# Kernel optimization log

Hardware: AMD Instinct MI355X
Metric: run time of the kernel (lower is better)

## Reference

```python
import jax, jax.numpy as jnp
import numpy as np

NEG_INF = -jnp.inf


def _bilinear_resize(x, out_h, out_w):
    """Matches torch F.interpolate(mode='bilinear', align_corners=False, antialias=False).
    x: [N, C, H, W] -> [N, C, out_h, out_w]."""
    N, C, H, W = x.shape

    def idx(in_s, out_s):
        scale = in_s / out_s
        src = jnp.maximum((jnp.arange(out_s, dtype=jnp.float32) + 0.5) * scale - 0.5, 0.0)
        i0 = jnp.floor(src).astype(jnp.int32)
        i1 = jnp.minimum(i0 + 1, in_s - 1)
        w = src - i0.astype(jnp.float32)
        return i0, i1, w

    y0, y1, wy = idx(H, out_h)
    x0, x1, wx = idx(W, out_w)
    # blend rows
    top = x[:, :, y0, :] * (1.0 - wy)[None, None, :, None] + x[:, :, y1, :] * wy[None, None, :, None]
    # blend cols
    out = top[:, :, :, x0] * (1.0 - wx)[None, None, None, :] + top[:, :, :, x1] * wx[None, None, None, :]
    return out


def _maxpool2(x):
    return jax.lax.reduce_window(x, NEG_INF, jax.lax.max,
                                 (1, 1, 2, 2), (1, 1, 2, 2), 'VALID')


def _lrelu(x):
    return jnp.where(x >= 0, x, 0.2 * x)


def setup_inputs() -> dict:
    key = jax.random.key(0)
    ks = jax.random.split(key, 6)
    N, C, H, W = 4, 32, 256, 256
    KS2 = 9
    psf = jax.random.normal(ks[0], (N, C, H, W), dtype=jnp.float32)
    featuremap = jax.random.normal(ks[1], (N, C, H, W), dtype=jnp.float32)
    w1 = jax.random.normal(ks[2], (C * KS2, C), dtype=jnp.float32) * 0.05
    b1 = jnp.zeros((C * KS2,), dtype=jnp.float32)
    ws = jax.random.normal(ks[3], (C * KS2, C), dtype=jnp.float32) * 0.05
    bs = jnp.zeros((C * KS2,), dtype=jnp.float32)
    return {"psf": psf, "featuremap": featuremap, "w1": w1, "b1": b1, "ws": ws, "bs": bs}


def reference(psf, featuremap, w1, b1, ws, bs):
    N, C, H, W = featuremap.shape
    KS = 3
    # psf branch: 1/4 bilinear -> maxpool2 -> KPResBlock (1x1 convs) -> x8 bilinear
    p = _bilinear_resize(psf, H // 4, W // 4)
    p = _maxpool2(p)                       # [N, C, H/8, W/8]
    identity = jnp.einsum('nchw,oc->nohw', p, ws) + bs[None, :, None, None]
    y = _lrelu(jnp.einsum('nchw,oc->nohw', p, w1) + b1[None, :, None, None]) + identity
    filt = _bilinear_resize(y, H, W)       # [N, C*9, H, W]
    # FAC: per-pixel dynamic 3x3 filter, fused (no materialized unfold)
    wflt = filt.reshape(N, C, KS * KS, H, W)
    padded = jnp.pad(featuremap, ((0, 0), (0, 0), (1, 1), (1, 1)))
    out = jnp.zeros((N, C, H, W), dtype=featuremap.dtype)
    for dy in range(KS):
        for dx in range(KS):
            out = out + padded[:, :, dy:dy + H, dx:dx + W] * wflt[:, :, dy * KS + dx]
    return out
```

## Files before the change

kernel.cpp:

```cpp
#include <hip/hip_runtime.h>

#define N_ 4
#define C_ 32
#define H_ 256
#define W_ 256
#define O_ 288
#define PH 32
#define P_ELEMS (N_*C_*PH*PH)
#define Y_ELEMS (N_*O_*PH*PH)
#define OUT_ELEMS (N_*C_*H_*W_)

__global__ __launch_bounds__(256) void k_downsample(
    const float* __restrict__ psf, float* __restrict__ p) {
  int tid = blockIdx.x * blockDim.x + threadIdx.x;
  if (tid >= P_ELEMS) return;
  int tx = tid & 31;
  int ty = (tid >> 5) & 31;
  int nc = tid >> 10;
  const float* x = psf + (size_t)nc * (H_ * W_);
  float m = -1e30f;
#pragma unroll
  for (int a = 0; a < 2; a++) {
#pragma unroll
    for (int b = 0; b < 2; b++) {
      int r0 = 8 * ty + 4 * a + 1;
      int c0 = 8 * tx + 4 * b;
      const float4 q0 = *(const float4*)(x + r0 * W_ + c0);
      const float4 q1 = *(const float4*)(x + (r0 + 1) * W_ + c0);
      float avg = 0.25f * (q0.y + q0.z + q1.y + q1.z);
      m = fmaxf(m, avg);
    }
  }
  p[tid] = m;
}

__global__ __launch_bounds__(256) void k_conv1x1(
    const float* __restrict__ p, const float* __restrict__ w1,
    const float* __restrict__ b1, const float* __restrict__ ws,
    const float* __restrict__ bs, float* __restrict__ y) {
  int bid = blockIdx.x;
  int n = bid / O_;
  int o = bid - n * O_;
  const float4* p4 = (const float4*)(p + (size_t)n * (C_ * PH * PH));
  const float* w1o = w1 + o * C_;
  const float* wso = ws + o * C_;
  float bb1 = b1[o];
  float bbs = bs[o];
  int t = threadIdx.x;
  float a1x = bb1, a1y = bb1, a1z = bb1, a1w = bb1;
  float a2x = bbs, a2y = bbs, a2z = bbs, a2w = bbs;
#pragma unroll
  for (int c = 0; c < C_; c++) {
    float4 pv = p4[c * 256 + t];
    float u1 = w1o[c], u2 = wso[c];
    a1x = fmaf(pv.x, u1, a1x); a1y = fmaf(pv.y, u1, a1y);
    a1z = fmaf(pv.z, u1, a1z); a1w = fmaf(pv.w, u1, a1w);
    a2x = fmaf(pv.x, u2, a2x); a2y = fmaf(pv.y, u2, a2y);
    a2z = fmaf(pv.z, u2, a2z); a2w = fmaf(pv.w, u2, a2w);
  }
  float4 r;
  r.x = ((a1x >= 0.f) ? a1x : 0.2f * a1x) + a2x;
  r.y = ((a1y >= 0.f) ? a1y : 0.2f * a1y) + a2y;
  r.z = ((a1z >= 0.f) ? a1z : 0.2f * a1z) + a2z;
  r.w = ((a1w >= 0.f) ? a1w : 0.2f * a1w) + a2w;
  ((float4*)(y + (size_t)bid * (PH * PH)))[t] = r;
}

__global__ __launch_bounds__(256) void k_fac(
    const float* __restrict__ fm, const float* __restrict__ y,
    float* __restrict__ out) {
  int bid = blockIdx.x;
  int work = (bid >> 3) + (bid & 7) * 256;
  int a = work & 15;
  int c = (work >> 4) & 31;
  int n = work >> 9;
  int t = threadIdx.x;
  int m = t & 31;
  int r = t >> 5;
  int h0 = (a << 4) + (r << 1);

  float sh0 = fmaxf(0.125f * (float)h0 - 0.4375f, 0.f);
  float sh1 = fmaxf(0.125f * (float)h0 - 0.3125f, 0.f);
  int y0 = (int)sh0;
  float wy0 = sh0 - (float)y0;
  float wy1 = sh1 - (float)y0;
  int y1 = min(y0 + 1, 31);

  const float* yb = y + ((size_t)(n * O_ + c * 9) << 10) + m;
  const float* yr0 = yb + (y0 << 5);
  const float* yr1 = yb + (y1 << 5);
  float tbA[9], tbB[9];
#pragma unroll
  for (int k = 0; k < 9; k++) {
    float t0 = yr0[k << 10];
    float u0 = yr1[k << 10];
    float d = u0 - t0;
    tbA[k] = fmaf(wy0, d, t0);
    tbB[k] = fmaf(wy1, d, t0);
  }
  int cm1 = max(m - 1, 0);
  int cp1 = min(m + 1, 31);

  const float* fb = fm + ((size_t)(n * C_ + c) << 16);

  float acc[16];
#pragma unroll
  for (int j = 0; j < 16; j++) acc[j] = 0.f;

#pragma unroll
  for (int i = 0; i < 4; i++) {
    int row = h0 - 1 + i;
    float fv[10];
    if (row >= 0 && row < 256) {
      const float* fr = fb + (row << 8) + (m << 3);
      float4 q0 = *(const float4*)(fr);
      float4 q1 = *(const float4*)(fr + 4);
      float left = __shfl(q1.w, cm1, 32);
      float right = __shfl(q0.x, cp1, 32);
      fv[0] = (m > 0) ? left : 0.f;
      fv[1] = q0.x; fv[2] = q0.y; fv[3] = q0.z; fv[4] = q0.w;
      fv[5] = q1.x; fv[6] = q1.y; fv[7] = q1.z; fv[8] = q1.w;
      fv[9] = (m < 31) ? right : 0.f;
    } else {
#pragma unroll
      for (int tt = 0; tt < 10; tt++) fv[tt] = 0.f;
    }
#pragma unroll
    for (int kx = 0; kx < 3; kx++) {
      if (i <= 2) {
        int k = 3 * i + kx;
        float tbm = tbA[k];
        float tbl = __shfl(tbm, cm1, 32);
        float tbr = __shfl(tbm, cp1, 32);
        float d0 = tbm - tbl;
        float d1 = tbr - tbm;
        acc[0] = fmaf(fv[0 + kx], fmaf(0.5625f, d0, tbl), acc[0]);
        acc[1] = fmaf(fv[1 + kx], fmaf(0.6875f, d0, tbl), acc[1]);
        acc[2] = fmaf(fv[2 + kx], fmaf(0.8125f, d0, tbl), acc[2]);
        acc[3] = fmaf(fv[3 + kx], fmaf(0.9375f, d0, tbl), acc[3]);
        acc[4] = fmaf(fv[4 + kx], fmaf(0.0625f, d1, tbm), acc[4]);
        acc[5] = fmaf(fv[5 + kx], fmaf(0.1875f, d1, tbm), acc[5]);
        acc[6] = fmaf(fv[6 + kx], fmaf(0.3125f, d1, tbm), acc[6]);
        acc[7] = fmaf(fv[7 + kx], fmaf(0.4375f, d1, tbm), acc[7]);
      }
      if (i >= 1) {
        int k = 3 * (i - 1) + kx;
        float tbm = tbB[k];
        float tbl = __shfl(tbm, cm1, 32);
        float tbr = __shfl(tbm, cp1, 32);
        float d0 = tbm - tbl;
        float d1 = tbr - tbm;
        acc[8]  = fmaf(fv[0 + kx], fmaf(0.5625f, d0, tbl), acc[8]);
        acc[9]  = fmaf(fv[1 + kx], fmaf(0.6875f, d0, tbl), acc[9]);
        acc[10] = fmaf(fv[2 + kx], fmaf(0.8125f, d0, tbl), acc[10]);
        acc[11] = fmaf(fv[3 + kx], fmaf(0.9375f, d0, tbl), acc[11]);
        acc[12] = fmaf(fv[4 + kx], fmaf(0.0625f, d1, tbm), acc[12]);
        acc[13] = fmaf(fv[5 + kx], fmaf(0.1875f, d1, tbm), acc[13]);
        acc[14] = fmaf(fv[6 + kx], fmaf(0.3125f, d1, tbm), acc[14]);
        acc[15] = fmaf(fv[7 + kx], fmaf(0.4375f, d1, tbm), acc[15]);
      }
    }
  }
  float* ob = out + ((size_t)(((n * C_ + c) << 8) + h0) << 8) + (m << 3);
  float4 r0 = {acc[0], acc[1], acc[2], acc[3]};
  float4 r1 = {acc[4], acc[5], acc[6], acc[7]};
  float4 r2 = {acc[8], acc[9], acc[10], acc[11]};
  float4 r3 = {acc[12], acc[13], acc[14], acc[15]};
  *(float4*)(ob) = r0;
  *(float4*)(ob + 4) = r1;
  *(float4*)(ob + 256) = r2;
  *(float4*)(ob + 260) = r3;
}

extern "C" void kernel_launch(void* const* d_in, const int* in_sizes, int n_in,
                              void* d_out, int out_size, void* d_ws,
                              size_t ws_size, hipStream_t stream) {
  const float* psf = (const float*)d_in[0];
  const float* fm = (const float*)d_in[1];
  const float* w1 = (const float*)d_in[2];
  const float* b1 = (const float*)d_in[3];
  const float* ws = (const float*)d_in[4];
  const float* bs = (const float*)d_in[5];
  float* out = (float*)d_out;

  float* p = (float*)d_ws;
  float* y = p + P_ELEMS;

  k_downsample<<<P_ELEMS / 256, 256, 0, stream>>>(psf, p);
  k_conv1x1<<<N_ * O_, 256, 0, stream>>>(p, w1, b1, ws, bs, y);
  k_fac<<<OUT_ELEMS / (16 * 256), 256, 0, stream>>>(fm, y, out);
}
```

Baseline: 123.5 us.

## Fuse 1x1 conv into FAC kernel computing needed filter rows in shared memory

Removes the separate conv1x1 kernel and the global y intermediate. Each FAC block now computes the 9x4x32 slice of filter coefficients it needs, for its channel and row band, into shared memory before the dynamic filtering. This saves one launch and the y write/read round trip. In exchange it recomputes overlapping rows across adjacent blocks and adds two barriers.

```diff
diff --git a/kernel.cpp b/kernel.cpp
--- a/kernel.cpp
+++ b/kernel.cpp
@@ -7,7 +7,6 @@
 #define O_ 288
 #define PH 32
 #define P_ELEMS (N_*C_*PH*PH)
-#define Y_ELEMS (N_*O_*PH*PH)
 #define OUT_ELEMS (N_*C_*H_*W_)
 
 __global__ __launch_bounds__(256) void k_downsample(
@@ -34,47 +33,66 @@
   p[tid] = m;
 }
 
-__global__ __launch_bounds__(256) void k_conv1x1(
+__global__ __launch_bounds__(256) void k_fused(
     const float* __restrict__ p, const float* __restrict__ w1,
     const float* __restrict__ b1, const float* __restrict__ ws,
-    const float* __restrict__ bs, float* __restrict__ y) {
-  int bid = blockIdx.x;
-  int n = bid / O_;
-  int o = bid - n * O_;
-  const float4* p4 = (const float4*)(p + (size_t)n * (C_ * PH * PH));
-  const float* w1o = w1 + o * C_;
-  const float* wso = ws + o * C_;
-  float bb1 = b1[o];
-  float bbs = bs[o];
-  int t = threadIdx.x;
-  float a1x = bb1, a1y = bb1, a1z = bb1, a1w = bb1;
-  float a2x = bbs, a2y = bbs, a2z = bbs, a2w = bbs;
-#pragma unroll
-  for (int c = 0; c < C_; c++) {
-    float4 pv = p4[c * 256 + t];
-    float u1 = w1o[c], u2 = wso[c];
-    a1x = fmaf(pv.x, u1, a1x); a1y = fmaf(pv.y, u1, a1y);
-    a1z = fmaf(pv.z, u1, a1z); a1w = fmaf(pv.w, u1, a1w);
-    a2x = fmaf(pv.x, u2, a2x); a2y = fmaf(pv.y, u2, a2y);
-    a2z = fmaf(pv.z, u2, a2z); a2w = fmaf(pv.w, u2, a2w);
-  }
-  float4 r;
-  r.x = ((a1x >= 0.f) ? a1x : 0.2f * a1x) + a2x;
-  r.y = ((a1y >= 0.f) ? a1y : 0.2f * a1y) + a2y;
-  r.z = ((a1z >= 0.f) ? a1z : 0.2f * a1z) + a2z;
-  r.w = ((a1w >= 0.f) ? a1w : 0.2f * a1w) + a2w;
-  ((float4*)(y + (size_t)bid * (PH * PH)))[t] = r;
-}
-
-__global__ __launch_bounds__(256) void k_fac(
-    const float* __restrict__ fm, const float* __restrict__ y,
+    const float* __restrict__ bs, const float* __restrict__ fm,
     float* __restrict__ out) {
+  __shared__ float w1_s[288];
+  __shared__ float ws_s[288];
+  __shared__ float y_tile[9][4][32];
+
   int bid = blockIdx.x;
   int work = (bid >> 3) + (bid & 7) * 256;
   int a = work & 15;
   int c = (work >> 4) & 31;
   int n = work >> 9;
   int t = threadIdx.x;
+  int row_base = 2 * a - 1;
+
+  {
+    const float* w1b = w1 + (size_t)c * 9 * 32;
+    const float* wsb = ws + (size_t)c * 9 * 32;
+    w1_s[t] = w1b[t];
+    ws_s[t] = wsb[t];
+    if (t < 32) {
+      w1_s[256 + t] = w1b[256 + t];
+      ws_s[256 + t] = wsb[256 + t];
+    }
+  }
+  __syncthreads();
+
+  {
+    auto conv_item = [&](int k, int j, int c4) {
+      int pr = min(max(row_base + j, 0), 31);
+      const float4* pp = (const float4*)p + ((size_t)n * (C_ * 256)) +
+                         (pr << 3) + c4;
+      int o = c * 9 + k;
+      float bb1 = b1[o], bbs = bs[o];
+      float a1x = bb1, a1y = bb1, a1z = bb1, a1w = bb1;
+      float a2x = bbs, a2y = bbs, a2z = bbs, a2w = bbs;
+#pragma unroll
+      for (int ch = 0; ch < C_; ch++) {
+        float4 pv = pp[ch << 8];
+        float u1 = w1_s[(k << 5) + ch];
+        float u2 = ws_s[(k << 5) + ch];
+        a1x = fmaf(pv.x, u1, a1x); a1y = fmaf(pv.y, u1, a1y);
+        a1z = fmaf(pv.z, u1, a1z); a1w = fmaf(pv.w, u1, a1w);
+        a2x = fmaf(pv.x, u2, a2x); a2y = fmaf(pv.y, u2, a2y);
+        a2z = fmaf(pv.z, u2, a2z); a2w = fmaf(pv.w, u2, a2w);
+      }
+      float4 rr;
+      rr.x = ((a1x >= 0.f) ? a1x : 0.2f * a1x) + a2x;
+      rr.y = ((a1y >= 0.f) ? a1y : 0.2f * a1y) + a2y;
+      rr.z = ((a1z >= 0.f) ? a1z : 0.2f * a1z) + a2z;
+      rr.w = ((a1w >= 0.f) ? a1w : 0.2f * a1w) + a2w;
+      *(float4*)&y_tile[k][j][c4 << 2] = rr;
+    };
+    conv_item(t >> 5, (t >> 3) & 3, t & 7);
+    if ((t & 63) < 8) conv_item(8, t >> 6, t & 7);
+  }
+  __syncthreads();
+
   int m = t & 31;
   int r = t >> 5;
   int h0 = (a << 4) + (r << 1);
@@ -84,16 +102,13 @@
   int y0 = (int)sh0;
   float wy0 = sh0 - (float)y0;
   float wy1 = sh1 - (float)y0;
-  int y1 = min(y0 + 1, 31);
-
-  const float* yb = y + ((size_t)(n * O_ + c * 9) << 10) + m;
-  const float* yr0 = yb + (y0 << 5);
-  const float* yr1 = yb + (y1 << 5);
+  int y0l = y0 - row_base;
+
   float tbA[9], tbB[9];
 #pragma unroll
   for (int k = 0; k < 9; k++) {
-    float t0 = yr0[k << 10];
-    float u0 = yr1[k << 10];
+    float t0 = y_tile[k][y0l][m];
+    float u0 = y_tile[k][y0l + 1][m];
     float d = u0 - t0;
     tbA[k] = fmaf(wy0, d, t0);
     tbB[k] = fmaf(wy1, d, t0);
@@ -184,9 +199,7 @@
   float* out = (float*)d_out;
 
   float* p = (float*)d_ws;
-  float* y = p + P_ELEMS;
 
   k_downsample<<<P_ELEMS / 256, 256, 0, stream>>>(psf, p);
-  k_conv1x1<<<N_ * O_, 256, 0, stream>>>(p, w1, b1, ws, bs, y);
-  k_fac<<<OUT_ELEMS / (16 * 256), 256, 0, stream>>>(fm, y, out);
+  k_fused<<<OUT_ELEMS / (16 * 256), 256, 0, stream>>>(p, w1, b1, ws, bs, fm, out);
 }
```

New measurement: 124.9 us. About the same (+1.1%).
